# Kernel optimization log

Measured on AMD Instinct MI355X. Metric: run time of the kernel, lower is better.

The kernel has to match this reference:

```python
import jax, jax.numpy as jnp
import numpy as np
from jax import lax

EXPANDED_BASE_DIM = 256
VISUAL_FEATURE_DIM = 768
HIDDEN_DIM = 1024
INPUT_DIM = EXPANDED_BASE_DIM + VISUAL_FEATURE_DIM
B, K = 256, 128


def setup_inputs() -> dict:
    key = jax.random.key(0)
    k1, k2, k3, k4, k5, k6 = jax.random.split(key, 6)
    s = 1.0 / np.sqrt(HIDDEN_DIM)  # PyTorch GRU init scale
    return {
        "base_expanded_seq": jax.random.normal(k1, (B, K, EXPANDED_BASE_DIM), jnp.float32),
        "visual_seq": jax.random.normal(k2, (B, K, VISUAL_FEATURE_DIM), jnp.float32),
        # PyTorch layout: gates stacked as [r, z, n] along first axis (3H)
        "W_ih": jax.random.uniform(k3, (3 * HIDDEN_DIM, INPUT_DIM), jnp.float32, -s, s),
        "W_hh": jax.random.uniform(k4, (3 * HIDDEN_DIM, HIDDEN_DIM), jnp.float32, -s, s),
        "b_ih": jax.random.uniform(k5, (3 * HIDDEN_DIM,), jnp.float32, -s, s),
        "b_hh": jax.random.uniform(k6, (3 * HIDDEN_DIM,), jnp.float32, -s, s),
    }


def reference(base_expanded_seq, visual_seq, W_ih, W_hh, b_ih, b_hh):
    # Faithful to GRUEncoder.forward: per-step concat -> GRU cell, return final h.
    x_seq = jnp.concatenate([base_expanded_seq, visual_seq], axis=-1)  # (B,K,I)
    Bb, Kk, _ = x_seq.shape
    H = W_hh.shape[1]
    # Precompute input projections for all steps (same math, batched GEMM)
    x_proj = jnp.einsum('bki,gi->bkg', x_seq, W_ih) + b_ih  # (B,K,3H)
    x_proj_t = jnp.swapaxes(x_proj, 0, 1)  # (K,B,3H)

    def step(h, xp):
        hp = h @ W_hh.T + b_hh  # (B,3H)
        xr, xz, xn = jnp.split(xp, 3, axis=-1)
        hr, hz, hn = jnp.split(hp, 3, axis=-1)
        r = jax.nn.sigmoid(xr + hr)
        z = jax.nn.sigmoid(xz + hz)
        n = jnp.tanh(xn + r * hn)
        h_new = (1.0 - z) * n + z * h
        return h_new, None

    h0 = jnp.zeros((Bb, H), x_seq.dtype)
    h_final, _ = lax.scan(step, h0, x_proj_t)
    return h_final  # (B, H) == h[-1] for num_layers=1
```

## Files before the change

kernel.cpp:

```cpp
#include <hip/hip_runtime.h>

#define BATCH 256
#define SEQ   128
#define IDIM  1024
#define HDIM  1024
#define G3    3072
#define RS    100

typedef __attribute__((ext_vector_type(8))) short bf16x8;
typedef __attribute__((ext_vector_type(4))) short s16x4;
typedef __attribute__((ext_vector_type(4))) float f32x4;

__device__ __forceinline__ short f2bf(float f) {
    union { float f; unsigned u; } x; x.f = f;
    unsigned r = x.u + 0x7fffu + ((x.u >> 16) & 1u);
    return (short)(r >> 16);
}
__device__ __forceinline__ float bf2f(unsigned short u) {
    union { unsigned u; float f; } x; x.u = ((unsigned)u) << 16;
    return x.f;
}

__device__ __forceinline__ void st_llc_b64(short* p, s16x4 v) {
    asm volatile("global_store_dwordx2 %0, %1, off sc0 sc1" :: "v"(p), "v"(v) : "memory");
}
__device__ __forceinline__ void st_llc_b32(unsigned* p, unsigned v) {
    asm volatile("global_store_dword %0, %1, off sc0 sc1" :: "v"(p), "v"(v) : "memory");
}
#define LDH(dst, p, OFF) \
    asm volatile("global_load_dwordx4 %0, %1, off offset:" OFF " sc0 sc1" \
                 : "=v"(dst) : "v"(p))
#define LDX(dst, p) \
    asm volatile("global_load_dwordx2 %0, %1, off" : "=v"(dst) : "v"(p))

__global__ void cvt_w(const float* __restrict__ wih, const float* __restrict__ whh,
                      short* __restrict__ wihb, short* __restrict__ whhb) {
    int i = blockIdx.x * 256 + threadIdx.x;
    const float* s; short* d; int j;
    if (i < 786432) { s = wih; d = wihb; j = i; }
    else            { s = whh; d = whhb; j = i - 786432; }
    const float4 v = *((const float4*)s + j);
    s16x4 o;
    o[0] = f2bf(v.x); o[1] = f2bf(v.y); o[2] = f2bf(v.z); o[3] = f2bf(v.w);
    *(s16x4*)(d + (size_t)j * 4) = o;
}

__global__ __launch_bounds__(256, 2) void gemm_xproj(
    const float* __restrict__ base, const float* __restrict__ vis,
    const short* __restrict__ wihb, const float* __restrict__ bih,
    short* __restrict__ xp)
{
    __shared__ union {
        struct { short A[128 * 64]; short B[128 * 64]; } ab;
        short C[128 * 136];
    } sm;
    const int tid = threadIdx.x;
    const int bid = blockIdx.x;
    const int nt = bid % 24, mt = bid / 24;
    const int m0 = mt * 128, n0 = nt * 128;
    const int lane = tid & 63, w = tid >> 6;
    const int wm = w >> 1, wn = w & 1;
    const int l15 = lane & 15, quad = lane >> 4;

    f32x4 acc[4][4];
#pragma unroll
    for (int i = 0; i < 4; ++i)
#pragma unroll
        for (int j = 0; j < 4; ++j) acc[i][j] = (f32x4){0.f, 0.f, 0.f, 0.f};

    const int arow = tid >> 3;
    const int acol8 = (tid & 7) * 8;

    for (int kt = 0; kt < 16; ++kt) {
        const int k0 = kt * 64;
        __syncthreads();
#pragma unroll
        for (int is = 0; is < 4; ++is) {
            const int row = is * 32 + arow;
            const int col = k0 + acol8;
            const float* s = (col < 256)
                ? (base + (size_t)(m0 + row) * 256 + col)
                : (vis  + (size_t)(m0 + row) * 768 + (col - 256));
            const float4 v0 = *(const float4*)s;
            const float4 v1 = *(const float4*)(s + 4);
            bf16x8 pk;
            pk[0] = f2bf(v0.x); pk[1] = f2bf(v0.y); pk[2] = f2bf(v0.z); pk[3] = f2bf(v0.w);
            pk[4] = f2bf(v1.x); pk[5] = f2bf(v1.y); pk[6] = f2bf(v1.z); pk[7] = f2bf(v1.w);
            *(bf16x8*)&sm.ab.A[is * 2048 + tid * 8] = pk;
            __builtin_amdgcn_global_load_lds(
                (const __attribute__((address_space(1))) void*)(wihb + (size_t)(n0 + is * 32 + (tid >> 3)) * 1024 + k0 + (tid & 7) * 8),
                (__attribute__((address_space(3))) void*)&sm.ab.B[is * 2048 + tid * 8],
                16, 0, 0);
        }
        __syncthreads();
#pragma unroll
        for (int s2 = 0; s2 < 2; ++s2) {
            bf16x8 af[4], bf[4];
#pragma unroll
            for (int i = 0; i < 4; ++i)
                af[i] = *(const bf16x8*)&sm.ab.A[(wm * 64 + i * 16 + l15) * 64 + s2 * 32 + quad * 8];
#pragma unroll
            for (int j = 0; j < 4; ++j)
                bf[j] = *(const bf16x8*)&sm.ab.B[(wn * 64 + j * 16 + l15) * 64 + s2 * 32 + quad * 8];
#pragma unroll
            for (int i = 0; i < 4; ++i)
#pragma unroll
                for (int j = 0; j < 4; ++j)
                    acc[i][j] = __builtin_amdgcn_mfma_f32_16x16x32_bf16(af[i], bf[j], acc[i][j], 0, 0, 0);
        }
    }
    __syncthreads();
#pragma unroll
    for (int j = 0; j < 4; ++j) {
        const int cn = wn * 64 + j * 16 + l15;
        const float bv = bih[n0 + cn];
#pragma unroll
        for (int i = 0; i < 4; ++i) {
            const int rb = wm * 64 + i * 16 + quad * 4;
#pragma unroll
            for (int r = 0; r < 4; ++r)
                sm.C[(rb + r) * 136 + cn] = f2bf(acc[i][j][r] + bv);
        }
    }
    __syncthreads();
    {
        const int row = tid >> 1, c0 = (tid & 1) * 64;
        const int gm = m0 + row;
        short* dst = xp + ((size_t)(gm & 127) * 256 + (size_t)(gm >> 7)) * 3072 + n0 + c0;
        const short* src = &sm.C[row * 136 + c0];
#pragma unroll
        for (int c = 0; c < 64; c += 8)
            *(bf16x8*)(dst + c) = *(const bf16x8*)(src + c);
    }
}

__global__ __launch_bounds__(256, 1) void gru_rec(
    const short* __restrict__ xp, const short* __restrict__ whhb,
    const float* __restrict__ bhh, short* __restrict__ hbuf,
    float* __restrict__ out, unsigned* __restrict__ flags)
{
    __shared__ float red[128 * RS];
    const int tid = threadIdx.x;
    const int bid = blockIdx.x;
    const int bt = bid >> 5;
    const int ct = bid & 31;
    const int lane = tid & 63, w = tid >> 6;
    const int l15 = lane & 15, quad = lane >> 4;
    const int bm0 = bt * 32;
    const int kbase = w * 256 + quad * 8;

    bf16x8 Bf[6][8];
#pragma unroll
    for (int g = 0; g < 6; ++g) {
        const size_t col = (size_t)((g >> 1) * 1024 + ct * 32 + (g & 1) * 16 + l15);
#pragma unroll
        for (int kk = 0; kk < 8; ++kk)
            Bf[g][kk] = *(const bf16x8*)(whhb + col * 1024 + kbase + kk * 32);
    }

    const int er = tid >> 3;
    const int ec0 = (tid & 7) * 4;
    const f32x4 bhr = *(const f32x4*)(bhh + ct * 32 + ec0);
    const f32x4 bhz = *(const f32x4*)(bhh + 1024 + ct * 32 + ec0);
    const f32x4 bhn = *(const f32x4*)(bhh + 2048 + ct * 32 + ec0);

    unsigned* const myflag = flags + bt * 32 + ct;
    const unsigned* const pollp = flags + bt * 32 + (lane & 31);

    float hold[4] = {0.f, 0.f, 0.f, 0.f};
    s16x4 xc[3], xn_[3];
    {
        const size_t rb = (size_t)(bm0 + er) * 3072 + ct * 32 + ec0;
#pragma unroll
        for (int g = 0; g < 3; ++g) xc[g] = *(const s16x4*)(xp + rb + g * 1024);
    }

    for (int step = 0; step < 128; ++step) {
        if (step > 0) {
            const unsigned tgt = (unsigned)step;
            unsigned fv;
            do {
                asm volatile("global_load_dword %0, %1, off sc0 sc1" : "=v"(fv) : "v"(pollp));
                asm volatile("s_waitcnt vmcnt(0)" : "+v"(fv) :: "memory");
            } while (__ballot(fv < tgt));
        }
        const short* hr_ = hbuf + (size_t)(step & 1) * (256 * 1024);
        short* hw_ = hbuf + (size_t)((step + 1) & 1) * (256 * 1024);

        bf16x8 A0[8], A1[8];
        const short* p0 = hr_ + (size_t)(bm0 + l15) * 1024 + kbase;
        const short* p1 = p0 + 16 * 1024;
        LDH(A0[0], p0, "0");   LDH(A0[1], p0, "64");  LDH(A0[2], p0, "128"); LDH(A0[3], p0, "192");
        LDH(A0[4], p0, "256"); LDH(A0[5], p0, "320"); LDH(A0[6], p0, "384"); LDH(A0[7], p0, "448");
        LDH(A1[0], p1, "0");   LDH(A1[1], p1, "64");  LDH(A1[2], p1, "128"); LDH(A1[3], p1, "192");
        LDH(A1[4], p1, "256"); LDH(A1[5], p1, "320"); LDH(A1[6], p1, "384"); LDH(A1[7], p1, "448");
        asm volatile("s_waitcnt vmcnt(0)"
            : "+v"(A0[0]), "+v"(A0[1]), "+v"(A0[2]), "+v"(A0[3]),
              "+v"(A0[4]), "+v"(A0[5]), "+v"(A0[6]), "+v"(A0[7]),
              "+v"(A1[0]), "+v"(A1[1]), "+v"(A1[2]), "+v"(A1[3]),
              "+v"(A1[4]), "+v"(A1[5]), "+v"(A1[6]), "+v"(A1[7])
            :: "memory");
        if (step < 127) {
            const short* rb = xp + ((size_t)(step + 1) * 256 + bm0 + er) * 3072 + ct * 32 + ec0;
            LDX(xn_[0], rb); LDX(xn_[1], rb + 1024); LDX(xn_[2], rb + 2048);
        }

        f32x4 acc[2][6];
#pragma unroll
        for (int i = 0; i < 2; ++i)
#pragma unroll
            for (int g = 0; g < 6; ++g) acc[i][g] = (f32x4){0.f, 0.f, 0.f, 0.f};
#pragma unroll
        for (int kk = 0; kk < 8; ++kk) {
#pragma unroll
            for (int g = 0; g < 6; ++g) {
                acc[0][g] = __builtin_amdgcn_mfma_f32_16x16x32_bf16(A0[kk], Bf[g][kk], acc[0][g], 0, 0, 0);
                acc[1][g] = __builtin_amdgcn_mfma_f32_16x16x32_bf16(A1[kk], Bf[g][kk], acc[1][g], 0, 0, 0);
            }
        }
#pragma unroll
        for (int i = 0; i < 2; ++i)
#pragma unroll
            for (int g = 0; g < 6; ++g) {
                const int c96 = (g >> 1) * 32 + (g & 1) * 16 + l15;
                const int rb = w * 32 + i * 16 + quad * 4;
#pragma unroll
                for (int r = 0; r < 4; ++r)
                    red[(rb + r) * RS + c96] = acc[i][g][r];
            }
        __syncthreads();
        f32x4 sr = bhr, sz = bhz, sn = bhn;
#pragma unroll
        for (int ww = 0; ww < 4; ++ww) {
            const float* rbp = &red[(ww * 32 + er) * RS];
            sr += *(const f32x4*)(rbp + ec0);
            sz += *(const f32x4*)(rbp + 32 + ec0);
            sn += *(const f32x4*)(rbp + 64 + ec0);
        }
        s16x4 hpk;
#pragma unroll
        for (int i = 0; i < 4; ++i) {
            const float xr = bf2f((unsigned short)xc[0][i]);
            const float xz = bf2f((unsigned short)xc[1][i]);
            const float xnv = bf2f((unsigned short)xc[2][i]);
            const float rg = 1.f / (1.f + __expf(-(xr + sr[i])));
            const float zg = 1.f / (1.f + __expf(-(xz + sz[i])));
            const float e2 = __expf(2.f * (xnv + rg * sn[i]));
            const float ng = 1.f - 2.f / (e2 + 1.f);
            const float hv = (1.f - zg) * ng + zg * hold[i];
            hold[i] = hv;
            hpk[i] = f2bf(hv);
        }
        if (step < 127) {
            st_llc_b64(&hw_[(size_t)(bm0 + er) * 1024 + ct * 32 + ec0], hpk);
            asm volatile("s_waitcnt vmcnt(0)"
                : "+v"(xn_[0]), "+v"(xn_[1]), "+v"(xn_[2]) :: "memory");
            __syncthreads();
            if (tid == 0) st_llc_b32(myflag, (unsigned)(step + 1));
            xc[0] = xn_[0]; xc[1] = xn_[1]; xc[2] = xn_[2];
        } else {
            __syncthreads();
        }
    }
    float4 o4; o4.x = hold[0]; o4.y = hold[1]; o4.z = hold[2]; o4.w = hold[3];
    *(float4*)(out + (size_t)(bm0 + er) * 1024 + ct * 32 + ec0) = o4;
}

extern "C" void kernel_launch(void* const* d_in, const int* in_sizes, int n_in,
                              void* d_out, int out_size, void* d_ws, size_t ws_size,
                              hipStream_t stream) {
    (void)in_sizes; (void)n_in; (void)out_size; (void)ws_size;
    const float* base = (const float*)d_in[0];
    const float* vis  = (const float*)d_in[1];
    const float* wih  = (const float*)d_in[2];
    const float* whh  = (const float*)d_in[3];
    const float* bih  = (const float*)d_in[4];
    const float* bhh  = (const float*)d_in[5];

    char* ws = (char*)d_ws;
    short*    xp   = (short*)(ws + 0);
    short*    wihb = (short*)(ws + 201326592);
    short*    whhb = (short*)(ws + 207618048);
    short*    hbuf = (short*)(ws + 213909504);
    unsigned* flg  = (unsigned*)(ws + 214958080);

    hipMemsetAsync(hbuf, 0, 1048576, stream);
    hipMemsetAsync(flg, 0, 4096, stream);

    cvt_w<<<dim3(6144), dim3(256), 0, stream>>>(wih, whh, wihb, whhb);
    gemm_xproj<<<dim3(6144), dim3(256), 0, stream>>>(base, vis, wihb, bih, xp);
    gru_rec<<<dim3(256), dim3(256), 0, stream>>>(xp, whhb, bhh, hbuf, (float*)d_out, flg);
}
```

Before: 1.189 ms.

## Double-buffer input-projection GEMM with register prefetch and packed bf16 conversion

Restructures the x-projection GEMM main loop to use two LDS buffers. The A tile for step k+2 is prefetched into registers while step k+1 is staged into LDS and step k is computed, which cuts one barrier per iteration and overlaps global loads with MFMA work. The fp32-to-bf16 conversion now uses the hardware packed v_cvt_pk_bf16_f32 instruction instead of manual rounding. In exchange, LDS use doubles, which can reduce occupancy under launch_bounds(256,2), and register pressure rises. This GEMM is likely a small share of total time compared with the recurrent part.

Result: no change. 1.192 ms (+0.2%).

```diff
diff --git a/kernel.cpp b/kernel.cpp
--- a/kernel.cpp
+++ b/kernel.cpp
@@ -51,7 +51,7 @@
     short* __restrict__ xp)
 {
     __shared__ union {
-        struct { short A[128 * 64]; short B[128 * 64]; } ab;
+        struct { short A[2][128 * 64]; short B[2][128 * 64]; } ab;
         short C[128 * 136];
     } sm;
     const int tid = threadIdx.x;
@@ -71,45 +71,65 @@
     const int arow = tid >> 3;
     const int acol8 = (tid & 7) * 8;
 
+    float4 pv0[4], pv1[4];
+
+    auto issueA = [&](int kt) {
+        const int col = kt * 64 + acol8;
+#pragma unroll
+        for (int is = 0; is < 4; ++is) {
+            const int row = m0 + is * 32 + arow;
+            const float* s = (col < 256)
+                ? (base + (size_t)row * 256 + col)
+                : (vis  + (size_t)row * 768 + (col - 256));
+            pv0[is] = *(const float4*)s;
+            pv1[is] = *(const float4*)(s + 4);
+        }
+    };
+    auto stage = [&](int buf, int kt) {
+        const int k0 = kt * 64;
+#pragma unroll
+        for (int is = 0; is < 4; ++is) {
+            union { unsigned u[4]; bf16x8 v; } pk;
+            asm("v_cvt_pk_bf16_f32 %0, %1, %2" : "=v"(pk.u[0]) : "v"(pv0[is].x), "v"(pv0[is].y));
+            asm("v_cvt_pk_bf16_f32 %0, %1, %2" : "=v"(pk.u[1]) : "v"(pv0[is].z), "v"(pv0[is].w));
+            asm("v_cvt_pk_bf16_f32 %0, %1, %2" : "=v"(pk.u[2]) : "v"(pv1[is].x), "v"(pv1[is].y));
+            asm("v_cvt_pk_bf16_f32 %0, %1, %2" : "=v"(pk.u[3]) : "v"(pv1[is].z), "v"(pv1[is].w));
+            *(bf16x8*)&sm.ab.A[buf][is * 2048 + tid * 8] = pk.v;
+            __builtin_amdgcn_global_load_lds(
+                (const __attribute__((address_space(1))) void*)(wihb + (size_t)(n0 + is * 32 + arow) * 1024 + k0 + acol8),
+                (__attribute__((address_space(3))) void*)&sm.ab.B[buf][is * 2048 + tid * 8],
+                16, 0, 0);
+        }
+    };
+
+    issueA(0);
+    stage(0, 0);
+    issueA(1);
+    __syncthreads();
+
     for (int kt = 0; kt < 16; ++kt) {
-        const int k0 = kt * 64;
+        const int cur = kt & 1, nxt = cur ^ 1;
+        if (kt < 15) {
+            stage(nxt, kt + 1);
+            if (kt < 14) issueA(kt + 2);
+        }
+#pragma unroll
+        for (int s2 = 0; s2 < 2; ++s2) {
+            bf16x8 af[4], bfv[4];
+#pragma unroll
+            for (int i = 0; i < 4; ++i)
+                af[i] = *(const bf16x8*)&sm.ab.A[cur][(wm * 64 + i * 16 + l15) * 64 + s2 * 32 + quad * 8];
+#pragma unroll
+            for (int j = 0; j < 4; ++j)
+                bfv[j] = *(const bf16x8*)&sm.ab.B[cur][(wn * 64 + j * 16 + l15) * 64 + s2 * 32 + quad * 8];
+#pragma unroll
+            for (int i = 0; i < 4; ++i)
+#pragma unroll
+                for (int j = 0; j < 4; ++j)
+                    acc[i][j] = __builtin_amdgcn_mfma_f32_16x16x32_bf16(af[i], bfv[j], acc[i][j], 0, 0, 0);
+        }
         __syncthreads();
-#pragma unroll
-        for (int is = 0; is < 4; ++is) {
-            const int row = is * 32 + arow;
-            const int col = k0 + acol8;
-            const float* s = (col < 256)
-                ? (base + (size_t)(m0 + row) * 256 + col)
-                : (vis  + (size_t)(m0 + row) * 768 + (col - 256));
-            const float4 v0 = *(const float4*)s;
-            const float4 v1 = *(const float4*)(s + 4);
-            bf16x8 pk;
-            pk[0] = f2bf(v0.x); pk[1] = f2bf(v0.y); pk[2] = f2bf(v0.z); pk[3] = f2bf(v0.w);
-            pk[4] = f2bf(v1.x); pk[5] = f2bf(v1.y); pk[6] = f2bf(v1.z); pk[7] = f2bf(v1.w);
-            *(bf16x8*)&sm.ab.A[is * 2048 + tid * 8] = pk;
-            __builtin_amdgcn_global_load_lds(
-                (const __attribute__((address_space(1))) void*)(wihb + (size_t)(n0 + is * 32 + (tid >> 3)) * 1024 + k0 + (tid & 7) * 8),
-                (__attribute__((address_space(3))) void*)&sm.ab.B[is * 2048 + tid * 8],
-                16, 0, 0);
-        }
-        __syncthreads();
-#pragma unroll
-        for (int s2 = 0; s2 < 2; ++s2) {
-            bf16x8 af[4], bf[4];
-#pragma unroll
-            for (int i = 0; i < 4; ++i)
-                af[i] = *(const bf16x8*)&sm.ab.A[(wm * 64 + i * 16 + l15) * 64 + s2 * 32 + quad * 8];
-#pragma unroll
-            for (int j = 0; j < 4; ++j)
-                bf[j] = *(const bf16x8*)&sm.ab.B[(wn * 64 + j * 16 + l15) * 64 + s2 * 32 + quad * 8];
-#pragma unroll
-            for (int i = 0; i < 4; ++i)
-#pragma unroll
-                for (int j = 0; j < 4; ++j)
-                    acc[i][j] = __builtin_amdgcn_mfma_f32_16x16x32_bf16(af[i], bf[j], acc[i][j], 0, 0, 0);
-        }
-    }
-    __syncthreads();
+    }
 #pragma unroll
     for (int j = 0; j < 4; ++j) {
         const int cn = wn * 64 + j * 16 + l15;
```

## Fuse input projection GEMM into recurrent kernel, computing x-proj per step off critical path

Applied to the files above, without the earlier changes.

Removes the separate x-projection GEMM kernel and its 3H-wide bf16 intermediate, and instead converts the inputs to time-major bf16. The recurrent kernel then computes each step's input projection with MFMA, reading W_ih from global/L2, after publishing its h flag, so the work overlaps the wait on other blocks. This cuts the large intermediate write and read but adds per-step W_ih streaming and extra syncs inside the recurrence, which only 256 blocks run.

New measurement: 1.877 ms. +57.9%, slower.

```diff
diff --git a/kernel.cpp b/kernel.cpp
--- a/kernel.cpp
+++ b/kernel.cpp
@@ -2,9 +2,7 @@
 
 #define BATCH 256
 #define SEQ   128
-#define IDIM  1024
 #define HDIM  1024
-#define G3    3072
 #define RS    100
 
 typedef __attribute__((ext_vector_type(8))) short bf16x8;
@@ -16,10 +14,6 @@
     unsigned r = x.u + 0x7fffu + ((x.u >> 16) & 1u);
     return (short)(r >> 16);
 }
-__device__ __forceinline__ float bf2f(unsigned short u) {
-    union { unsigned u; float f; } x; x.u = ((unsigned)u) << 16;
-    return x.f;
-}
 
 __device__ __forceinline__ void st_llc_b64(short* p, s16x4 v) {
     asm volatile("global_store_dwordx2 %0, %1, off sc0 sc1" :: "v"(p), "v"(v) : "memory");
@@ -30,113 +24,40 @@
 #define LDH(dst, p, OFF) \
     asm volatile("global_load_dwordx4 %0, %1, off offset:" OFF " sc0 sc1" \
                  : "=v"(dst) : "v"(p))
-#define LDX(dst, p) \
-    asm volatile("global_load_dwordx2 %0, %1, off" : "=v"(dst) : "v"(p))
-
-__global__ void cvt_w(const float* __restrict__ wih, const float* __restrict__ whh,
-                      short* __restrict__ wihb, short* __restrict__ whhb) {
-    int i = blockIdx.x * 256 + threadIdx.x;
-    const float* s; short* d; int j;
-    if (i < 786432) { s = wih; d = wihb; j = i; }
-    else            { s = whh; d = whhb; j = i - 786432; }
-    const float4 v = *((const float4*)s + j);
-    s16x4 o;
-    o[0] = f2bf(v.x); o[1] = f2bf(v.y); o[2] = f2bf(v.z); o[3] = f2bf(v.w);
-    *(s16x4*)(d + (size_t)j * 4) = o;
-}
-
-__global__ __launch_bounds__(256, 2) void gemm_xproj(
-    const float* __restrict__ base, const float* __restrict__ vis,
-    const short* __restrict__ wihb, const float* __restrict__ bih,
-    short* __restrict__ xp)
-{
-    __shared__ union {
-        struct { short A[128 * 64]; short B[128 * 64]; } ab;
-        short C[128 * 136];
-    } sm;
-    const int tid = threadIdx.x;
-    const int bid = blockIdx.x;
-    const int nt = bid % 24, mt = bid / 24;
-    const int m0 = mt * 128, n0 = nt * 128;
-    const int lane = tid & 63, w = tid >> 6;
-    const int wm = w >> 1, wn = w & 1;
-    const int l15 = lane & 15, quad = lane >> 4;
-
-    f32x4 acc[4][4];
-#pragma unroll
-    for (int i = 0; i < 4; ++i)
-#pragma unroll
-        for (int j = 0; j < 4; ++j) acc[i][j] = (f32x4){0.f, 0.f, 0.f, 0.f};
-
-    const int arow = tid >> 3;
-    const int acol8 = (tid & 7) * 8;
-
-    for (int kt = 0; kt < 16; ++kt) {
-        const int k0 = kt * 64;
-        __syncthreads();
-#pragma unroll
-        for (int is = 0; is < 4; ++is) {
-            const int row = is * 32 + arow;
-            const int col = k0 + acol8;
-            const float* s = (col < 256)
-                ? (base + (size_t)(m0 + row) * 256 + col)
-                : (vis  + (size_t)(m0 + row) * 768 + (col - 256));
-            const float4 v0 = *(const float4*)s;
-            const float4 v1 = *(const float4*)(s + 4);
-            bf16x8 pk;
-            pk[0] = f2bf(v0.x); pk[1] = f2bf(v0.y); pk[2] = f2bf(v0.z); pk[3] = f2bf(v0.w);
-            pk[4] = f2bf(v1.x); pk[5] = f2bf(v1.y); pk[6] = f2bf(v1.z); pk[7] = f2bf(v1.w);
-            *(bf16x8*)&sm.ab.A[is * 2048 + tid * 8] = pk;
-            __builtin_amdgcn_global_load_lds(
-                (const __attribute__((address_space(1))) void*)(wihb + (size_t)(n0 + is * 32 + (tid >> 3)) * 1024 + k0 + (tid & 7) * 8),
-                (__attribute__((address_space(3))) void*)&sm.ab.B[is * 2048 + tid * 8],
-                16, 0, 0);
-        }
-        __syncthreads();
-#pragma unroll
-        for (int s2 = 0; s2 < 2; ++s2) {
-            bf16x8 af[4], bf[4];
-#pragma unroll
-            for (int i = 0; i < 4; ++i)
-                af[i] = *(const bf16x8*)&sm.ab.A[(wm * 64 + i * 16 + l15) * 64 + s2 * 32 + quad * 8];
-#pragma unroll
-            for (int j = 0; j < 4; ++j)
-                bf[j] = *(const bf16x8*)&sm.ab.B[(wn * 64 + j * 16 + l15) * 64 + s2 * 32 + quad * 8];
-#pragma unroll
-            for (int i = 0; i < 4; ++i)
-#pragma unroll
-                for (int j = 0; j < 4; ++j)
-                    acc[i][j] = __builtin_amdgcn_mfma_f32_16x16x32_bf16(af[i], bf[j], acc[i][j], 0, 0, 0);
-        }
+
+__global__ void cvt_all(const float* __restrict__ wih, const float* __restrict__ whh,
+                        const float* __restrict__ base, const float* __restrict__ vis,
+                        short* __restrict__ wihb, short* __restrict__ whhb,
+                        short* __restrict__ xb) {
+    const int i = blockIdx.x * 256 + threadIdx.x;
+    if (i < 1572864) {
+        const float* s; short* d; int j;
+        if (i < 786432) { s = wih; d = wihb; j = i; }
+        else            { s = whh; d = whhb; j = i - 786432; }
+        const float4 v = *((const float4*)s + j);
+        s16x4 o;
+        o[0] = f2bf(v.x); o[1] = f2bf(v.y); o[2] = f2bf(v.z); o[3] = f2bf(v.w);
+        *(s16x4*)(d + (size_t)j * 4) = o;
+    } else {
+        const int j = i - 1572864;
+        const int e0 = j * 4;
+        const int r = e0 >> 10;
+        const int c = e0 & 1023;
+        const int b = r & 255, k = r >> 8;
+        const float* s = (c < 256)
+            ? (base + (size_t)(b * 128 + k) * 256 + c)
+            : (vis  + (size_t)(b * 128 + k) * 768 + (c - 256));
+        const float4 v = *(const float4*)s;
+        s16x4 o;
+        o[0] = f2bf(v.x); o[1] = f2bf(v.y); o[2] = f2bf(v.z); o[3] = f2bf(v.w);
+        *(s16x4*)(xb + (size_t)e0) = o;
     }
-    __syncthreads();
-#pragma unroll
-    for (int j = 0; j < 4; ++j) {
-        const int cn = wn * 64 + j * 16 + l15;
-        const float bv = bih[n0 + cn];
-#pragma unroll
-        for (int i = 0; i < 4; ++i) {
-            const int rb = wm * 64 + i * 16 + quad * 4;
-#pragma unroll
-            for (int r = 0; r < 4; ++r)
-                sm.C[(rb + r) * 136 + cn] = f2bf(acc[i][j][r] + bv);
-        }
-    }
-    __syncthreads();
-    {
-        const int row = tid >> 1, c0 = (tid & 1) * 64;
-        const int gm = m0 + row;
-        short* dst = xp + ((size_t)(gm & 127) * 256 + (size_t)(gm >> 7)) * 3072 + n0 + c0;
-        const short* src = &sm.C[row * 136 + c0];
-#pragma unroll
-        for (int c = 0; c < 64; c += 8)
-            *(bf16x8*)(dst + c) = *(const bf16x8*)(src + c);
-    }
 }
 
 __global__ __launch_bounds__(256, 1) void gru_rec(
-    const short* __restrict__ xp, const short* __restrict__ whhb,
-    const float* __restrict__ bhh, short* __restrict__ hbuf,
+    const short* __restrict__ xb,   const short* __restrict__ wihb,
+    const short* __restrict__ whhb, const float* __restrict__ bih,
+    const float* __restrict__ bhh,  short* __restrict__ hbuf,
     float* __restrict__ out, unsigned* __restrict__ flags)
 {
     __shared__ float red[128 * RS];
@@ -150,9 +71,11 @@
     const int kbase = w * 256 + quad * 8;
 
     bf16x8 Bf[6][8];
+    const short* wp[6];
 #pragma unroll
     for (int g = 0; g < 6; ++g) {
         const size_t col = (size_t)((g >> 1) * 1024 + ct * 32 + (g & 1) * 16 + l15);
+        wp[g] = wihb + col * 1024 + kbase;
 #pragma unroll
         for (int kk = 0; kk < 8; ++kk)
             Bf[g][kk] = *(const bf16x8*)(whhb + col * 1024 + kbase + kk * 32);
@@ -163,17 +86,62 @@
     const f32x4 bhr = *(const f32x4*)(bhh + ct * 32 + ec0);
     const f32x4 bhz = *(const f32x4*)(bhh + 1024 + ct * 32 + ec0);
     const f32x4 bhn = *(const f32x4*)(bhh + 2048 + ct * 32 + ec0);
+    const f32x4 bir = *(const f32x4*)(bih + ct * 32 + ec0);
+    const f32x4 biz = *(const f32x4*)(bih + 1024 + ct * 32 + ec0);
+    const f32x4 bin_ = *(const f32x4*)(bih + 2048 + ct * 32 + ec0);
 
     unsigned* const myflag = flags + bt * 32 + ct;
     const unsigned* const pollp = flags + bt * 32 + (lane & 31);
 
     float hold[4] = {0.f, 0.f, 0.f, 0.f};
-    s16x4 xc[3], xn_[3];
-    {
-        const size_t rb = (size_t)(bm0 + er) * 3072 + ct * 32 + ec0;
-#pragma unroll
-        for (int g = 0; g < 3; ++g) xc[g] = *(const s16x4*)(xp + rb + g * 1024);
-    }
+    bf16x8 A0[8], A1[8];
+    f32x4 acc[2][6];
+    f32x4 xg[3];
+
+    auto XP = [&](int t) {
+        const short* xa0 = xb + ((size_t)(t * 256 + bm0 + l15)) * 1024 + kbase;
+        const short* xa1 = xa0 + 16 * 1024;
+#pragma unroll
+        for (int kk = 0; kk < 8; ++kk) {
+            A0[kk] = *(const bf16x8*)(xa0 + kk * 32);
+            A1[kk] = *(const bf16x8*)(xa1 + kk * 32);
+        }
+#pragma unroll
+        for (int i = 0; i < 2; ++i)
+#pragma unroll
+            for (int g = 0; g < 6; ++g) acc[i][g] = (f32x4){0.f, 0.f, 0.f, 0.f};
+#pragma unroll
+        for (int kk = 0; kk < 8; ++kk) {
+#pragma unroll
+            for (int g = 0; g < 6; ++g) {
+                const bf16x8 wf = *(const bf16x8*)(wp[g] + kk * 32);
+                acc[0][g] = __builtin_amdgcn_mfma_f32_16x16x32_bf16(A0[kk], wf, acc[0][g], 0, 0, 0);
+                acc[1][g] = __builtin_amdgcn_mfma_f32_16x16x32_bf16(A1[kk], wf, acc[1][g], 0, 0, 0);
+            }
+        }
+#pragma unroll
+        for (int i = 0; i < 2; ++i)
+#pragma unroll
+            for (int g = 0; g < 6; ++g) {
+                const int c96 = (g >> 1) * 32 + (g & 1) * 16 + l15;
+                const int rb = w * 32 + i * 16 + quad * 4;
+#pragma unroll
+                for (int r = 0; r < 4; ++r)
+                    red[(rb + r) * RS + c96] = acc[i][g][r];
+            }
+        __syncthreads();
+        xg[0] = bir; xg[1] = biz; xg[2] = bin_;
+#pragma unroll
+        for (int ww = 0; ww < 4; ++ww) {
+            const float* rbp = &red[(ww * 32 + er) * RS];
+            xg[0] += *(const f32x4*)(rbp + ec0);
+            xg[1] += *(const f32x4*)(rbp + 32 + ec0);
+            xg[2] += *(const f32x4*)(rbp + 64 + ec0);
+        }
+        __syncthreads();
+    };
+
+    XP(0);
 
     for (int step = 0; step < 128; ++step) {
         if (step > 0) {
@@ -187,25 +155,15 @@
         const short* hr_ = hbuf + (size_t)(step & 1) * (256 * 1024);
         short* hw_ = hbuf + (size_t)((step + 1) & 1) * (256 * 1024);
 
-        bf16x8 A0[8], A1[8];
         const short* p0 = hr_ + (size_t)(bm0 + l15) * 1024 + kbase;
         const short* p1 = p0 + 16 * 1024;
         LDH(A0[0], p0, "0");   LDH(A0[1], p0, "64");  LDH(A0[2], p0, "128"); LDH(A0[3], p0, "192");
         LDH(A0[4], p0, "256"); LDH(A0[5], p0, "320"); LDH(A0[6], p0, "384"); LDH(A0[7], p0, "448");
         LDH(A1[0], p1, "0");   LDH(A1[1], p1, "64");  LDH(A1[2], p1, "128"); LDH(A1[3], p1, "192");
         LDH(A1[4], p1, "256"); LDH(A1[5], p1, "320"); LDH(A1[6], p1, "384"); LDH(A1[7], p1, "448");
-        asm volatile("s_waitcnt vmcnt(0)"
-            : "+v"(A0[0]), "+v"(A0[1]), "+v"(A0[2]), "+v"(A0[3]),
-              "+v"(A0[4]), "+v"(A0[5]), "+v"(A0[6]), "+v"(A0[7]),
-              "+v"(A1[0]), "+v"(A1[1]), "+v"(A1[2]), "+v"(A1[3]),
-              "+v"(A1[4]), "+v"(A1[5]), "+v"(A1[6]), "+v"(A1[7])
-            :: "memory");
-        if (step < 127) {
-            const short* rb = xp + ((size_t)(step + 1) * 256 + bm0 + er) * 3072 + ct * 32 + ec0;
-            LDX(xn_[0], rb); LDX(xn_[1], rb + 1024); LDX(xn_[2], rb + 2048);
-        }
-
-        f32x4 acc[2][6];
+        asm volatile("s_waitcnt vmcnt(0)" ::: "memory");
+        __builtin_amdgcn_sched_barrier(0);
+
 #pragma unroll
         for (int i = 0; i < 2; ++i)
 #pragma unroll
@@ -240,9 +198,9 @@
         s16x4 hpk;
 #pragma unroll
         for (int i = 0; i < 4; ++i) {
-            const float xr = bf2f((unsigned short)xc[0][i]);
-            const float xz = bf2f((unsigned short)xc[1][i]);
-            const float xnv = bf2f((unsigned short)xc[2][i]);
+            const float xr = xg[0][i];
+            const float xz = xg[1][i];
+            const float xnv = xg[2][i];
             const float rg = 1.f / (1.f + __expf(-(xr + sr[i])));
             const float zg = 1.f / (1.f + __expf(-(xz + sz[i])));
             const float e2 = __expf(2.f * (xnv + rg * sn[i]));
@@ -253,11 +211,11 @@
         }
         if (step < 127) {
             st_llc_b64(&hw_[(size_t)(bm0 + er) * 1024 + ct * 32 + ec0], hpk);
-            asm volatile("s_waitcnt vmcnt(0)"
-                : "+v"(xn_[0]), "+v"(xn_[1]), "+v"(xn_[2]) :: "memory");
+            asm volatile("s_waitcnt vmcnt(0)" ::: "memory");
+            __builtin_amdgcn_sched_barrier(0);
             __syncthreads();
             if (tid == 0) st_llc_b32(myflag, (unsigned)(step + 1));
-            xc[0] = xn_[0]; xc[1] = xn_[1]; xc[2] = xn_[2];
+            XP(step + 1);
         } else {
             __syncthreads();
         }
@@ -278,16 +236,16 @@
     const float* bhh  = (const float*)d_in[5];
 
     char* ws = (char*)d_ws;
-    short*    xp   = (short*)(ws + 0);
+    short*    xb   = (short*)(ws + 0);
     short*    wihb = (short*)(ws + 201326592);
     short*    whhb = (short*)(ws + 207618048);
     short*    hbuf = (short*)(ws + 213909504);
     unsigned* flg  = (unsigned*)(ws + 214958080);
 
-    hipMemsetAsync(hbuf, 0, 1048576, stream);
-    hipMemsetAsync(flg, 0, 4096, stream);
-
-    cvt_w<<<dim3(6144), dim3(256), 0, stream>>>(wih, whh, wihb, whhb);
-    gemm_xproj<<<dim3(6144), dim3(256), 0, stream>>>(base, vis, wihb, bih, xp);
-    gru_rec<<<dim3(256), dim3(256), 0, stream>>>(xp, whhb, bhh, hbuf, (float*)d_out, flg);
-}
+    (void)hipMemsetAsync(hbuf, 0, 1048576, stream);
+    (void)hipMemsetAsync(flg, 0, 4096, stream);
+
+    cvt_all<<<dim3(38912), dim3(256), 0, stream>>>(wih, whh, base, vis, wihb, whhb, xb);
+    gru_rec<<<dim3(256), dim3(256), 0, stream>>>(xb, wihb, whhb, bih, bhh, hbuf,
+                                                 (float*)d_out, flg);
+}
```
